# Kernel tuning notes

Hardware: AMD Instinct MI355X
Metric: run time of the kernel (lower is better)

The kernel has to match this reference:

```python
import jax, jax.numpy as jnp
import numpy as np

S = 10       # speakers (== num nodes N, per module construction)
D = 1024     # hidden_dim
R = 2 * S * S  # num_relations


def _forward(global_features, speaker, Wq, Wk, rgcn_weight, rgcn_root,
             rgcn_bias, gcn_rel_w, gcn_rel_b, gcn_root_w):
    N, d = global_features.shape
    # ---- single-head global attention -> edge weights (softmax over keys) ----
    # keys are the node features themselves (stacked N times in the original)
    q = global_features @ Wq                       # [N, D]
    k = global_features @ Wk                       # [N, D]
    attn = jax.nn.softmax((q @ k.T) / jnp.sqrt(jnp.asarray(d, q.dtype)), axis=-1)  # [N, N]

    # ---- dense all-pairs edge list, row-major (i, j) like itertools product ----
    src = jnp.repeat(jnp.arange(N), N)             # edge_index[0]
    dst = jnp.tile(jnp.arange(N), N)               # edge_index[1]
    edge_weight = attn.reshape(-1)                 # matches torch.flatten order

    # edge_type id = 2*(s_i*S + s_j) + direction, direction = 0 if i<j else 1
    etype = 2 * (speaker[src] * S + speaker[dst]) + (src >= dst).astype(speaker.dtype)

    # ---- RGCN with per-relation MEAN aggregation (PyG RGCNConv default) ----
    # mean is per (relation, dst-node) over weighted messages; transform is linear
    # so we fold weight[rel] into each edge and normalize by segment counts.
    seg = etype * N + dst                           # (relation, dst) segment id
    cnt = jax.ops.segment_sum(jnp.ones_like(edge_weight), seg, num_segments=R * N)
    w_e = edge_weight / cnt[seg]                    # cnt >= 1 on every live edge
    # per-edge gather of relation weight + matmul: [E, D] x [E, D, D] -> [E, D]
    msg = w_e[:, None] * jnp.einsum('ed,edf->ef', global_features[src], rgcn_weight[etype])
    out = jax.ops.segment_sum(msg, dst, num_segments=N)    # scatter-add to dst
    out = out + global_features @ rgcn_root + rgcn_bias    # root + bias

    # ---- GraphConv (sum aggregation, no edge weight): lin_rel(agg) + lin_root(x) ----
    agg = jax.ops.segment_sum(out[src], dst, num_segments=N)
    x2 = agg @ gcn_rel_w + gcn_rel_b + out @ gcn_root_w

    return jnp.concatenate([x2, global_features], axis=-1)  # [N, 2D]


def setup_inputs() -> dict:
    key = jax.random.key(0)
    ks = jax.random.split(key, 10)
    scale = 0.02
    return {
        'global_features': jax.random.normal(ks[0], (S, D), dtype=jnp.float32),
        'speaker': jax.random.randint(ks[1], (S,), 0, S, dtype=jnp.int32),
        'Wq': jax.random.normal(ks[2], (D, D), dtype=jnp.float32) * scale,
        'Wk': jax.random.normal(ks[3], (D, D), dtype=jnp.float32) * scale,
        'rgcn_weight': jax.random.normal(ks[4], (R, D, D), dtype=jnp.float32) * scale,
        'rgcn_root': jax.random.normal(ks[5], (D, D), dtype=jnp.float32) * scale,
        'rgcn_bias': jax.random.normal(ks[6], (D,), dtype=jnp.float32) * scale,
        'gcn_rel_w': jax.random.normal(ks[7], (D, D), dtype=jnp.float32) * scale,
        'gcn_rel_b': jax.random.normal(ks[8], (D,), dtype=jnp.float32) * scale,
        'gcn_root_w': jax.random.normal(ks[9], (D, D), dtype=jnp.float32) * scale,
    }


def reference(global_features, speaker, Wq, Wk, rgcn_weight, rgcn_root,
              rgcn_bias, gcn_rel_w, gcn_rel_b, gcn_root_w):
    return _forward(global_features, speaker, Wq, Wk, rgcn_weight, rgcn_root,
                    rgcn_bias, gcn_rel_w, gcn_rel_b, gcn_root_w)
```

## Files before the change

kernel.cpp:

```cpp
#include <hip/hip_runtime.h>

#define N 10
#define D 1024
#define NREL 200
#define KCH 32
#define KLEN 32

typedef float f32x4 __attribute__((ext_vector_type(4)));

#define OFF_Q       0
#define OFF_K       (OFF_Q + N*D)
#define OFF_OUTACC  (OFF_K + N*D)
#define OFF_X2ACC   (OFF_OUTACC + N*D)
#define OFF_AGGREL  (OFF_X2ACC + N*D)
#define ZERO_FLOATS (OFF_AGGREL + D)
#define OFF_WE      ZERO_FLOATS
#define OFF_ETYPE   (OFF_WE + 128)

__device__ __forceinline__ void matvec_body(const float* __restrict__ x,
                                            const float* __restrict__ W,
                                            float* __restrict__ y,
                                            int c, int kb) {
    const float* Wp = W + (size_t)kb * D + c;
    const float* xp = x + kb;
    float acc = 0.f;
#pragma unroll 8
    for (int k = 0; k < 128; ++k) acc += xp[k] * Wp[(size_t)k * D];
    atomicAdd(&y[c], acc);
}

__global__ void pre_matvec(const float* __restrict__ X, const float* __restrict__ Wq,
                           const float* __restrict__ Wk, const float* __restrict__ Wroot,
                           float* __restrict__ q, float* __restrict__ kout,
                           float* __restrict__ outacc) {
    int r   = blockIdx.x % N;
    int sel = blockIdx.x / N;
    const float* W = (sel == 0) ? Wq : (sel == 1) ? Wk : Wroot;
    float*       Y = (sel == 0) ? q  : (sel == 1) ? kout : outacc;
    matvec_body(X + r * D, W, Y + r * D, blockIdx.y * 256 + threadIdx.x, blockIdx.z * 128);
}

__global__ void attn_edges(const float* __restrict__ q, const float* __restrict__ k,
                           const int* __restrict__ speaker, const float* __restrict__ bias,
                           float* __restrict__ w_e, int* __restrict__ etype_out,
                           float* __restrict__ outacc) {
    __shared__ float logits[N * N];
    __shared__ float attn[N * N];
    __shared__ int   cnt[NREL * N];
    int tid  = threadIdx.x;
    int wave = tid >> 6, lane = tid & 63;

    for (int p = wave; p < N * N; p += 16) {
        int i = p / N, j = p % N;
        const f32x4* qp = reinterpret_cast<const f32x4*>(q + i * D);
        const f32x4* kp = reinterpret_cast<const f32x4*>(k + j * D);
        float acc = 0.f;
#pragma unroll
        for (int it = 0; it < 4; ++it) {
            f32x4 qa = qp[lane + it * 64];
            f32x4 ka = kp[lane + it * 64];
            acc += qa.x * ka.x + qa.y * ka.y + qa.z * ka.z + qa.w * ka.w;
        }
        for (int off = 32; off; off >>= 1) acc += __shfl_down(acc, off);
        if (lane == 0) logits[p] = acc * (1.0f / 32.0f);
    }
    for (int i = tid; i < N * D; i += 1024) outacc[i] += bias[i & (D - 1)];
    __syncthreads();

    if (tid < N) {
        float m = -1e30f;
        for (int j = 0; j < N; ++j) m = fmaxf(m, logits[tid * N + j]);
        float s = 0.f, e[N];
        for (int j = 0; j < N; ++j) { e[j] = expf(logits[tid * N + j] - m); s += e[j]; }
        for (int j = 0; j < N; ++j) attn[tid * N + j] = e[j] / s;
    }
    for (int i = tid; i < NREL * N; i += 1024) cnt[i] = 0;
    __syncthreads();

    if (tid < N * N) {
        int src = tid / N, dst = tid % N;
        int et  = 2 * (speaker[src] * N + speaker[dst]) + (src >= dst ? 1 : 0);
        etype_out[tid] = et;
        atomicAdd(&cnt[et * N + dst], 1);
    }
    __syncthreads();

    if (tid < N * N) {
        int dst = tid % N;
        w_e[tid] = attn[tid] / (float)cnt[etype_out[tid] * N + dst];
    }
}

__global__ void edge_matvec(const float* __restrict__ X, const float* __restrict__ Wr,
                            const float* __restrict__ w_e, const int* __restrict__ etype,
                            float* __restrict__ outacc) {
    int e   = blockIdx.x;
    int kc  = blockIdx.y;
    int src = e / N, dst = e % N;
    int t   = etype[e];
    float we = w_e[e];
    const float* W = Wr + (size_t)t * D * D + (size_t)kc * KLEN * D;
    const float* x = X + src * D + kc * KLEN;
    int c0 = threadIdx.x * 4;
    f32x4 acc = 0.f;
#pragma unroll 8
    for (int k = 0; k < KLEN; ++k) {
        f32x4 w4 = __builtin_nontemporal_load(
            reinterpret_cast<const f32x4*>(W + (size_t)k * D + c0));
        acc += x[k] * w4;
    }
    float* o = outacc + dst * D + c0;
    atomicAdd(o + 0, we * acc.x);
    atomicAdd(o + 1, we * acc.y);
    atomicAdd(o + 2, we * acc.z);
    atomicAdd(o + 3, we * acc.w);
}

__global__ void final_matvec(const float* __restrict__ outacc,
                             const float* __restrict__ root_w, const float* __restrict__ rel_w,
                             float* __restrict__ x2acc, float* __restrict__ aggrel) {
    __shared__ float xs[128];
    int r  = blockIdx.x;
    int c  = blockIdx.y * 256 + threadIdx.x;
    int kb = blockIdx.z * 128;
    if (threadIdx.x < 128) {
        if (r < N) {
            xs[threadIdx.x] = outacc[r * D + kb + threadIdx.x];
        } else {
            float s = 0.f;
#pragma unroll
            for (int rr = 0; rr < N; ++rr) s += outacc[rr * D + kb + threadIdx.x];
            xs[threadIdx.x] = s;
        }
    }
    __syncthreads();
    const float* W = (r < N) ? root_w : rel_w;
    float*       y = (r < N) ? x2acc + r * D : aggrel;
    const float* Wp = W + (size_t)kb * D + c;
    float acc = 0.f;
#pragma unroll 8
    for (int k = 0; k < 128; ++k) acc += xs[k] * Wp[(size_t)k * D];
    atomicAdd(&y[c], acc);
}

__global__ void final_concat(const float* __restrict__ x2acc, const float* __restrict__ aggrel,
                             const float* __restrict__ rel_b, const float* __restrict__ X,
                             float* __restrict__ dout) {
    int r = blockIdx.x, c = blockIdx.y * 256 + threadIdx.x;
    if (c < D) dout[r * 2 * D + c] = x2acc[r * D + c] + aggrel[c] + rel_b[c];
    else       dout[r * 2 * D + c] = X[r * D + (c - D)];
}

extern "C" void kernel_launch(void* const* d_in, const int* in_sizes, int n_in,
                              void* d_out, int out_size, void* d_ws, size_t ws_size,
                              hipStream_t stream) {
    const float* X          = (const float*)d_in[0];
    const int*   speaker    = (const int*)  d_in[1];
    const float* Wq         = (const float*)d_in[2];
    const float* Wk         = (const float*)d_in[3];
    const float* Wrel       = (const float*)d_in[4];
    const float* Wroot      = (const float*)d_in[5];
    const float* bias       = (const float*)d_in[6];
    const float* gcn_rel_w  = (const float*)d_in[7];
    const float* gcn_rel_b  = (const float*)d_in[8];
    const float* gcn_root_w = (const float*)d_in[9];
    float* ws   = (float*)d_ws;
    float* dout = (float*)d_out;

    float* q      = ws + OFF_Q;
    float* kbuf   = ws + OFF_K;
    float* outacc = ws + OFF_OUTACC;
    float* x2acc  = ws + OFF_X2ACC;
    float* aggrel = ws + OFF_AGGREL;
    float* w_e    = ws + OFF_WE;
    int*   etype  = (int*)(ws + OFF_ETYPE);

    hipMemsetAsync(ws, 0, ZERO_FLOATS * sizeof(float), stream);

    dim3 blk(256);
    pre_matvec<<<dim3(3 * N, 4, 8), blk, 0, stream>>>(X, Wq, Wk, Wroot, q, kbuf, outacc);
    attn_edges<<<1, dim3(1024), 0, stream>>>(q, kbuf, speaker, bias, w_e, etype, outacc);

    edge_matvec<<<dim3(N * N, KCH), blk, 0, stream>>>(X, Wrel, w_e, etype, outacc);

    final_matvec<<<dim3(N + 1, 4, 8), blk, 0, stream>>>(outacc, gcn_root_w, gcn_rel_w,
                                                        x2acc, aggrel);
    final_concat<<<dim3(N, 8), blk, 0, stream>>>(x2acc, aggrel, gcn_rel_b, X, dout);
}
```

Measured before the change: 130.6 us.

## Group edges by relation to share weight loads and fuse projection matvecs

Adds a build_groups kernel that buckets the 100 edges by relation type, so each block streams one relation weight slice once and applies it to up to eight source vectors. Per-edge unweighted messages go to a new buffer, and the attention edge weights are applied later in combine_final, which takes edge weighting and bias off the critical path. The Q/K/root projections share the same launch and now process all ten rows per weight load instead of one. The cost is an extra serial single-block grouping kernel, a larger memset for the N*N*D message buffer, and extra reads of that buffer in the final stage.

Measured after the change: 128.6 us. Within noise of the previous version (-1.5%).

```diff
diff --git a/kernel.cpp b/kernel.cpp
--- a/kernel.cpp
+++ b/kernel.cpp
@@ -5,45 +5,127 @@
 #define NREL 200
 #define KCH 32
 #define KLEN 32
+#define MAXG 8
 
 typedef float f32x4 __attribute__((ext_vector_type(4)));
 
 #define OFF_Q       0
 #define OFF_K       (OFF_Q + N*D)
-#define OFF_OUTACC  (OFF_K + N*D)
-#define OFF_X2ACC   (OFF_OUTACC + N*D)
+#define OFF_ROOT    (OFF_K + N*D)
+#define OFF_X2ACC   (OFF_ROOT + N*D)
 #define OFF_AGGREL  (OFF_X2ACC + N*D)
-#define ZERO_FLOATS (OFF_AGGREL + D)
+#define OFF_EM      (OFF_AGGREL + D)
+#define ZERO_FLOATS (OFF_EM + N*N*D)
 #define OFF_WE      ZERO_FLOATS
-#define OFF_ETYPE   (OFF_WE + 128)
-
-__device__ __forceinline__ void matvec_body(const float* __restrict__ x,
-                                            const float* __restrict__ W,
-                                            float* __restrict__ y,
-                                            int c, int kb) {
-    const float* Wp = W + (size_t)kb * D + c;
-    const float* xp = x + kb;
-    float acc = 0.f;
-#pragma unroll 8
-    for (int k = 0; k < 128; ++k) acc += xp[k] * Wp[(size_t)k * D];
-    atomicAdd(&y[c], acc);
-}
-
-__global__ void pre_matvec(const float* __restrict__ X, const float* __restrict__ Wq,
-                           const float* __restrict__ Wk, const float* __restrict__ Wroot,
-                           float* __restrict__ q, float* __restrict__ kout,
-                           float* __restrict__ outacc) {
-    int r   = blockIdx.x % N;
-    int sel = blockIdx.x / N;
-    const float* W = (sel == 0) ? Wq : (sel == 1) ? Wk : Wroot;
-    float*       Y = (sel == 0) ? q  : (sel == 1) ? kout : outacc;
-    matvec_body(X + r * D, W, Y + r * D, blockIdx.y * 256 + threadIdx.x, blockIdx.z * 128);
+#define OFF_NITEMS  (OFF_WE + 128)
+#define OFF_ITEMS   (OFF_NITEMS + 16)
+
+__global__ void build_groups(const int* __restrict__ speaker, int* __restrict__ n_items,
+                             int* __restrict__ items) {
+    __shared__ int sp[N];
+    __shared__ int gcnt[NREL];
+    __shared__ int ibase[NREL];
+    int tid = threadIdx.x;
+    if (tid < N) sp[tid] = speaker[tid];
+    __syncthreads();
+    if (tid < NREL) {
+        int c = 0;
+        for (int e = 0; e < N * N; ++e) {
+            int src = e / N, dst = e % N;
+            int et = 2 * (sp[src] * N + sp[dst]) + (src >= dst ? 1 : 0);
+            c += (et == tid);
+        }
+        gcnt[tid] = c;
+    }
+    __syncthreads();
+    if (tid == 0) {
+        int b = 0;
+        for (int t = 0; t < NREL; ++t) { ibase[t] = b; b += (gcnt[t] + MAXG - 1) / MAXG; }
+        *n_items = b;
+    }
+    __syncthreads();
+    if (tid < NREL && gcnt[tid] > 0) {
+        int it = ibase[tid], slot = 0;
+        int* rec = items + it * 10;
+        for (int e = 0; e < N * N; ++e) {
+            int src = e / N, dst = e % N;
+            int et = 2 * (sp[src] * N + sp[dst]) + (src >= dst ? 1 : 0);
+            if (et != tid) continue;
+            if (slot == 0) rec[0] = tid;
+            rec[2 + slot] = e;
+            if (++slot == MAXG) { rec[1] = MAXG; ++it; rec = items + it * 10; slot = 0; }
+        }
+        if (slot > 0) { rec[1] = slot; for (int g = slot; g < MAXG; ++g) rec[2 + g] = -1; }
+    }
+}
+
+__global__ void big_fused(const float* __restrict__ X, const float* __restrict__ Wrel,
+                          const int* __restrict__ n_items, const int* __restrict__ items,
+                          const float* __restrict__ Wq, const float* __restrict__ Wk,
+                          const float* __restrict__ Wroot,
+                          float* __restrict__ q, float* __restrict__ kout,
+                          float* __restrict__ rootacc, float* __restrict__ em) {
+    int bx = blockIdx.x, by = blockIdx.y, tid = threadIdx.x;
+    if (bx < 100) {
+        if (bx >= *n_items) return;
+        __shared__ int   meta[10];
+        __shared__ float xs[MAXG][KLEN];
+        if (tid < 10) meta[tid] = items[bx * 10 + tid];
+        __syncthreads();
+        int t = meta[0], gsize = meta[1];
+        {
+            int g = tid >> 5, k = tid & 31;
+            int e = meta[2 + g];
+            xs[g][k] = (g < gsize) ? X[(e / N) * D + by * KLEN + k] : 0.f;
+        }
+        __syncthreads();
+        int c0 = tid * 4;
+        const float* W = Wrel + (size_t)t * D * D + (size_t)by * KLEN * D;
+        f32x4 acc[MAXG];
+#pragma unroll
+        for (int g = 0; g < MAXG; ++g) acc[g] = 0.f;
+#pragma unroll 4
+        for (int k = 0; k < KLEN; ++k) {
+            f32x4 w4 = __builtin_nontemporal_load(
+                reinterpret_cast<const f32x4*>(W + (size_t)k * D + c0));
+#pragma unroll
+            for (int g = 0; g < MAXG; ++g) acc[g] += xs[g][k] * w4;
+        }
+        for (int g = 0; g < gsize; ++g) {
+            float* o = em + (size_t)meta[2 + g] * D + c0;
+            atomicAdd(o + 0, acc[g].x);
+            atomicAdd(o + 1, acc[g].y);
+            atomicAdd(o + 2, acc[g].z);
+            atomicAdd(o + 3, acc[g].w);
+        }
+    } else {
+        int sel = bx - 100;
+        int kb  = (by & 7) * 128;
+        int c   = (by >> 3) * 256 + tid;
+        const float* W = (sel == 0) ? Wq : (sel == 1) ? Wk : Wroot;
+        float*       Y = (sel == 0) ? q  : (sel == 1) ? kout : rootacc;
+        __shared__ float xs2[N][128];
+        for (int idx = tid; idx < N * 128; idx += 256) {
+            int r = idx >> 7, k = idx & 127;
+            xs2[r][k] = X[r * D + kb + k];
+        }
+        __syncthreads();
+        float acc[N];
+#pragma unroll
+        for (int r = 0; r < N; ++r) acc[r] = 0.f;
+#pragma unroll 4
+        for (int k = 0; k < 128; ++k) {
+            float w = W[(size_t)(kb + k) * D + c];
+#pragma unroll
+            for (int r = 0; r < N; ++r) acc[r] += xs2[r][k] * w;
+        }
+#pragma unroll
+        for (int r = 0; r < N; ++r) atomicAdd(&Y[r * D + c], acc[r]);
+    }
 }
 
 __global__ void attn_edges(const float* __restrict__ q, const float* __restrict__ k,
-                           const int* __restrict__ speaker, const float* __restrict__ bias,
-                           float* __restrict__ w_e, int* __restrict__ etype_out,
-                           float* __restrict__ outacc) {
+                           const int* __restrict__ speaker, float* __restrict__ w_e) {
     __shared__ float logits[N * N];
     __shared__ float attn[N * N];
     __shared__ int   cnt[NREL * N];
@@ -64,7 +146,6 @@
         for (int off = 32; off; off >>= 1) acc += __shfl_down(acc, off);
         if (lane == 0) logits[p] = acc * (1.0f / 32.0f);
     }
-    for (int i = tid; i < N * D; i += 1024) outacc[i] += bias[i & (D - 1)];
     __syncthreads();
 
     if (tid < N) {
@@ -77,61 +158,48 @@
     for (int i = tid; i < NREL * N; i += 1024) cnt[i] = 0;
     __syncthreads();
 
+    int et = 0;
     if (tid < N * N) {
         int src = tid / N, dst = tid % N;
-        int et  = 2 * (speaker[src] * N + speaker[dst]) + (src >= dst ? 1 : 0);
-        etype_out[tid] = et;
+        et = 2 * (speaker[src] * N + speaker[dst]) + (src >= dst ? 1 : 0);
         atomicAdd(&cnt[et * N + dst], 1);
     }
     __syncthreads();
 
     if (tid < N * N) {
-        int dst = tid % N;
-        w_e[tid] = attn[tid] / (float)cnt[etype_out[tid] * N + dst];
-    }
-}
-
-__global__ void edge_matvec(const float* __restrict__ X, const float* __restrict__ Wr,
-                            const float* __restrict__ w_e, const int* __restrict__ etype,
-                            float* __restrict__ outacc) {
-    int e   = blockIdx.x;
-    int kc  = blockIdx.y;
-    int src = e / N, dst = e % N;
-    int t   = etype[e];
-    float we = w_e[e];
-    const float* W = Wr + (size_t)t * D * D + (size_t)kc * KLEN * D;
-    const float* x = X + src * D + kc * KLEN;
-    int c0 = threadIdx.x * 4;
-    f32x4 acc = 0.f;
-#pragma unroll 8
-    for (int k = 0; k < KLEN; ++k) {
-        f32x4 w4 = __builtin_nontemporal_load(
-            reinterpret_cast<const f32x4*>(W + (size_t)k * D + c0));
-        acc += x[k] * w4;
-    }
-    float* o = outacc + dst * D + c0;
-    atomicAdd(o + 0, we * acc.x);
-    atomicAdd(o + 1, we * acc.y);
-    atomicAdd(o + 2, we * acc.z);
-    atomicAdd(o + 3, we * acc.w);
-}
-
-__global__ void final_matvec(const float* __restrict__ outacc,
-                             const float* __restrict__ root_w, const float* __restrict__ rel_w,
-                             float* __restrict__ x2acc, float* __restrict__ aggrel) {
+        w_e[tid] = attn[tid] / (float)cnt[et * N + (tid % N)];
+    }
+}
+
+__global__ void combine_final(const float* __restrict__ em, const float* __restrict__ w_e,
+                              const float* __restrict__ rootacc, const float* __restrict__ bias,
+                              const float* __restrict__ root_w, const float* __restrict__ rel_w,
+                              float* __restrict__ x2acc, float* __restrict__ aggrel) {
+    __shared__ float wes[N * N];
     __shared__ float xs[128];
-    int r  = blockIdx.x;
-    int c  = blockIdx.y * 256 + threadIdx.x;
-    int kb = blockIdx.z * 128;
-    if (threadIdx.x < 128) {
+    int r   = blockIdx.x;
+    int tid = threadIdx.x;
+    int c   = blockIdx.y * 256 + tid;
+    int kb  = blockIdx.z * 128;
+    if (tid < N * N) wes[tid] = w_e[tid];
+    __syncthreads();
+    if (tid < 128) {
+        int j = kb + tid;
+        float v;
         if (r < N) {
-            xs[threadIdx.x] = outacc[r * D + kb + threadIdx.x];
+            v = rootacc[r * D + j] + bias[j];
+#pragma unroll
+            for (int src = 0; src < N; ++src) {
+                int e = src * N + r;
+                v += wes[e] * em[(size_t)e * D + j];
+            }
         } else {
-            float s = 0.f;
-#pragma unroll
-            for (int rr = 0; rr < N; ++rr) s += outacc[rr * D + kb + threadIdx.x];
-            xs[threadIdx.x] = s;
-        }
+            v = (float)N * bias[j];
+#pragma unroll
+            for (int rr = 0; rr < N; ++rr) v += rootacc[rr * D + j];
+            for (int e = 0; e < N * N; ++e) v += wes[e] * em[(size_t)e * D + j];
+        }
+        xs[tid] = v;
     }
     __syncthreads();
     const float* W = (r < N) ? root_w : rel_w;
@@ -167,23 +235,26 @@
     float* ws   = (float*)d_ws;
     float* dout = (float*)d_out;
 
-    float* q      = ws + OFF_Q;
-    float* kbuf   = ws + OFF_K;
-    float* outacc = ws + OFF_OUTACC;
-    float* x2acc  = ws + OFF_X2ACC;
-    float* aggrel = ws + OFF_AGGREL;
-    float* w_e    = ws + OFF_WE;
-    int*   etype  = (int*)(ws + OFF_ETYPE);
+    float* q       = ws + OFF_Q;
+    float* kbuf    = ws + OFF_K;
+    float* rootacc = ws + OFF_ROOT;
+    float* x2acc   = ws + OFF_X2ACC;
+    float* aggrel  = ws + OFF_AGGREL;
+    float* em      = ws + OFF_EM;
+    float* w_e     = ws + OFF_WE;
+    int*   nitems  = (int*)(ws + OFF_NITEMS);
+    int*   items   = (int*)(ws + OFF_ITEMS);
 
     hipMemsetAsync(ws, 0, ZERO_FLOATS * sizeof(float), stream);
 
     dim3 blk(256);
-    pre_matvec<<<dim3(3 * N, 4, 8), blk, 0, stream>>>(X, Wq, Wk, Wroot, q, kbuf, outacc);
-    attn_edges<<<1, dim3(1024), 0, stream>>>(q, kbuf, speaker, bias, w_e, etype, outacc);
-
-    edge_matvec<<<dim3(N * N, KCH), blk, 0, stream>>>(X, Wrel, w_e, etype, outacc);
-
-    final_matvec<<<dim3(N + 1, 4, 8), blk, 0, stream>>>(outacc, gcn_root_w, gcn_rel_w,
-                                                        x2acc, aggrel);
+    build_groups<<<1, blk, 0, stream>>>(speaker, nitems, items);
+
+    big_fused<<<dim3(103, KCH), blk, 0, stream>>>(X, Wrel, nitems, items, Wq, Wk, Wroot,
+                                                  q, kbuf, rootacc, em);
+
+    attn_edges<<<1, dim3(1024), 0, stream>>>(q, kbuf, speaker, w_e);
+    combine_final<<<dim3(N + 1, 4, 8), blk, 0, stream>>>(em, w_e, rootacc, bias,
+                                                         gcn_root_w, gcn_rel_w, x2acc, aggrel);
     final_concat<<<dim3(N, 8), blk, 0, stream>>>(x2acc, aggrel, gcn_rel_b, X, dout);
 }
```
